# Kernel optimization log

Measured on AMD Instinct MI355X. Metric: run time of the kernel, lower is better.

## Reference

```python
import jax, jax.numpy as jnp
import numpy as np

N_NODES = 200000
N_EDGES = 12800000
C = 5  # channels
RADIUS = 0.05
CONSUME_RADIUS = RADIUS * 2
ACCEL_SCALE = 0.01
MAX_VEL = 0.1
CONSUME_EDGES_REQ = 3
EDGES_TO_STAY_ALIVE = 1
NEG_SLOPE = 0.2  # GATConv leaky_relu slope


def setup_inputs() -> dict:
    key = jax.random.key(0)
    ks = jax.random.split(key, 16)
    x = jax.random.normal(ks[0], (N_NODES, C), dtype=jnp.float32) * 0.1
    # column 4 is node type: 1 = cell, 0 = food
    is_cell = jax.random.bernoulli(ks[1], 0.9, (N_NODES,)).astype(jnp.float32)
    x = x.at[:, 4].set(is_cell)
    edge_index = jax.random.randint(ks[2], (2, N_EDGES), 0, N_NODES, dtype=jnp.int32)
    # edge_attr: [distance, is_cell_edge]
    dist = jax.random.uniform(ks[3], (N_EDGES,), dtype=jnp.float32) * 0.2
    cell_edge = jax.random.bernoulli(ks[4], 0.8, (N_EDGES,)).astype(jnp.float32)
    edge_attr = jnp.stack([dist, cell_edge], axis=1)
    s = 1.0 / np.sqrt(C)
    W = jax.random.normal(ks[5], (C, C), dtype=jnp.float32) * s        # GAT lin (shared src/dst)
    att_src = jax.random.normal(ks[6], (C,), dtype=jnp.float32) * s
    att_dst = jax.random.normal(ks[7], (C,), dtype=jnp.float32) * s
    We = jax.random.normal(ks[8], (2, C), dtype=jnp.float32) * 0.7      # lin_edge
    att_edge = jax.random.normal(ks[9], (C,), dtype=jnp.float32) * s
    gat_bias = jnp.zeros((C,), dtype=jnp.float32)
    W1 = jax.random.normal(ks[10], (C, C), dtype=jnp.float32) * s
    b1 = jnp.zeros((C,), dtype=jnp.float32)
    W2 = jax.random.normal(ks[11], (C, 2), dtype=jnp.float32) * s
    b2 = jnp.zeros((2,), dtype=jnp.float32)
    return {"x": x, "edge_index": edge_index, "edge_attr": edge_attr,
            "W": W, "att_src": att_src, "att_dst": att_dst, "We": We,
            "att_edge": att_edge, "gat_bias": gat_bias,
            "W1": W1, "b1": b1, "W2": W2, "b2": b2}


def _gat_conv(x, edge_index, edge_attr, W, att_src, att_dst, We, att_edge, gat_bias):
    # PyG GATConv, heads=1, edge_dim=2: softmax over incoming edges of each dst node
    n = x.shape[0]
    src, dst = edge_index[0], edge_index[1]
    hs = x @ W                                   # [N, C]
    a_src = hs @ att_src                         # [N]
    a_dst = hs @ att_dst                         # [N]
    a_e = (edge_attr @ We) @ att_edge            # [E]
    logits = jax.nn.leaky_relu(a_src[src] + a_dst[dst] + a_e, NEG_SLOPE)  # [E]
    m = jax.ops.segment_max(logits, dst, num_segments=n)                  # [N]
    ev = jnp.exp(logits - m[dst])
    denom = jax.ops.segment_sum(ev, dst, num_segments=n)                  # [N]
    alpha = ev / jnp.maximum(denom, 1e-16)[dst]
    out = jax.ops.segment_sum(hs[src] * alpha[:, None], dst, num_segments=n)
    return out + gat_bias


def reference(x, edge_index, edge_attr, W, att_src, att_dst, We, att_edge, gat_bias, W1, b1, W2, b2):
    n = x.shape[0]
    src = edge_index[0]
    # convolve: GAT -> MLP -> *2-1
    h = _gat_conv(x, edge_index, edge_attr, W, att_src, att_dst, We, att_edge, gat_bias)
    h = jax.nn.relu(jax.nn.relu(h @ W1 + b1) @ W2 + b2)
    h = h * 2.0 - 1.0                             # [N, 2]
    # only cells (type==1) accelerate
    food_mask = (x[:, 4] == 1).astype(jnp.float32)
    accel = h * ACCEL_SCALE * food_mask[:, None]
    velocity = jnp.clip(x[:, 2:4] + accel, -MAX_VEL, MAX_VEL)
    positions = x[:, :2] + velocity
    new_x = jnp.concatenate([positions, velocity, x[:, 4:]], axis=1)  # [N, 5]
    # border cost
    eps = 1e-6
    out_mask = (jnp.abs(positions) > 1).astype(jnp.float32)
    border_cost = jnp.sum(jnp.log(jnp.abs(positions) + eps) * out_mask)
    # consume-food mask: food nodes with >=3 close edges
    close = (edge_attr[:, 0] < CONSUME_RADIUS).astype(jnp.int32)
    close_cnt = jax.ops.segment_sum(close, src, num_segments=n)
    consumed = (x[:, 4] == 0) & (close_cnt >= CONSUME_EDGES_REQ)
    # island-cell mask: cells with < 1 cell-edge
    cell_e = (edge_attr[:, 1] == 1).astype(jnp.int32)
    cell_cnt = jax.ops.segment_sum(cell_e, src, num_segments=n)
    dead = (x[:, 4] == 1) & (cell_cnt < EDGES_TO_STAY_ALIVE)
    return (new_x, jnp.mean(jnp.abs(velocity), axis=0), border_cost,
            jnp.sum(consumed.astype(jnp.int32)), jnp.sum(dead.astype(jnp.int32)))
```

## Files before the change

kernel.cpp:

```cpp
#include <hip/hip_runtime.h>
#include <math.h>

#define NEG_SLOPE   0.2f
#define CONSUME_R   0.1f
#define ACCEL_SCALE 0.01f
#define MAX_VEL     0.1f

#define NBUCK  2048
#define TPB    512
#define EPT    16
#define EPB    (TPB*EPT)
#define MAXNPB 128
#define SMAX   6912

typedef float    v2f __attribute__((ext_vector_type(2)));
typedef unsigned v2u __attribute__((ext_vector_type(2)));

__device__ __forceinline__ unsigned bucket_of(unsigned v, unsigned npb, float inv_npb,
                                              unsigned* loc)
{
    unsigned b = (unsigned)((float)v * inv_npb);
    unsigned lo = b * npb;
    if (v < lo)            { --b; lo -= npb; }
    else if (v >= lo + npb){ ++b; lo += npb; }
    *loc = v - lo;
    return b;
}

__global__ __launch_bounds__(256) void k_pre(
    const float* __restrict__ x, const float* __restrict__ W,
    const float* __restrict__ att_src, const float* __restrict__ att_dst,
    uint4* __restrict__ npack, float* __restrict__ aD, int n)
{
    int i = blockIdx.x * 256 + threadIdx.x;
    if (i >= n) return;
    float xr[5];
#pragma unroll
    for (int k = 0; k < 5; ++k) xr[k] = x[(size_t)i * 5 + k];
    float hs[5];
#pragma unroll
    for (int c = 0; c < 5; ++c) {
        float s = 0.f;
#pragma unroll
        for (int k = 0; k < 5; ++k) s += xr[k] * W[k * 5 + c];
        hs[c] = s;
    }
    float a_s = 0.f, a_d = 0.f;
#pragma unroll
    for (int c = 0; c < 5; ++c) { a_s += hs[c] * att_src[c]; a_d += hs[c] * att_dst[c]; }
    aD[i] = a_d;
    unsigned b[5];
#pragma unroll
    for (int c = 0; c < 5; ++c) {
        unsigned u = __float_as_uint(hs[c]);
        b[c] = (u + 0x7FFFu + ((u >> 16) & 1u)) >> 16;
    }
    npack[i] = make_uint4(b[0] | (b[1] << 16), b[2] | (b[3] << 16), b[4],
                          __float_as_uint(a_s));
}

__global__ __launch_bounds__(TPB) void k_hist(
    const int* __restrict__ dst, int* __restrict__ hist,
    int NB, int nE, unsigned npb, float inv_npb)
{
    __shared__ int hd[NBUCK];
    int t = threadIdx.x, blk = blockIdx.x;
    for (int j = t; j < NBUCK; j += TPB) hd[j] = 0;
    __syncthreads();
    int base = blk * EPB;
#pragma unroll 4
    for (int k = 0; k < EPT; ++k) {
        int e = base + k * TPB + t;
        if (e < nE) {
            unsigned loc;
            unsigned bd = bucket_of((unsigned)__builtin_nontemporal_load(dst + e),
                                    npb, inv_npb, &loc);
            atomicAdd(&hd[bd], 1);
        }
    }
    __syncthreads();
    for (int j = t; j < NBUCK; j += TPB) hist[(size_t)blk * NBUCK + j] = hd[j];
}

__global__ __launch_bounds__(256) void k_scanA(
    int* __restrict__ hist, int* __restrict__ rowtot, int NB)
{
    int b = blockIdx.x, t = threadIdx.x;
    __shared__ int ws4[4];
    __shared__ int carry;
    if (t == 0) carry = 0;
    __syncthreads();
    for (int base = 0; base < NB; base += 256) {
        int i = base + t;
        int v = (i < NB) ? hist[(size_t)i * NBUCK + b] : 0;
        int xv = v;
#pragma unroll
        for (int off = 1; off < 64; off <<= 1) {
            int y = __shfl_up(xv, off);
            if ((t & 63) >= off) xv += y;
        }
        if ((t & 63) == 63) ws4[t >> 6] = xv;
        __syncthreads();
        int add = 0;
        for (int w = 0; w < (t >> 6); ++w) add += ws4[w];
        int total = ws4[0] + ws4[1] + ws4[2] + ws4[3];
        if (i < NB) hist[(size_t)i * NBUCK + b] = carry + xv + add - v;
        __syncthreads();
        if (t == 0) carry += total;
        __syncthreads();
    }
    if (t == 0) rowtot[b] = carry;
}

__global__ __launch_bounds__(1024) void k_scanB(
    const int* __restrict__ rowtot, int* __restrict__ bbase)
{
    __shared__ int wsum[16], wex[16];
    int t = threadIdx.x;
    int a = rowtot[2 * t], b2 = rowtot[2 * t + 1];
    int v = a + b2;
    int xv = v;
#pragma unroll
    for (int off = 1; off < 64; off <<= 1) {
        int y = __shfl_up(xv, off);
        if ((t & 63) >= off) xv += y;
    }
    if ((t & 63) == 63) wsum[t >> 6] = xv;
    __syncthreads();
    if (t == 0) { int r = 0; for (int w = 0; w < 16; ++w) { wex[w] = r; r += wsum[w]; } }
    __syncthreads();
    int excl = xv - v + wex[t >> 6];
    bbase[2 * t] = excl;
    bbase[2 * t + 1] = excl + a;
    if (t == 1023) bbase[NBUCK] = excl + v;
}

__global__ __launch_bounds__(TPB) void k_scatter(
    const int* __restrict__ ei, const float* __restrict__ ea,
    const float* __restrict__ We, const float* __restrict__ att_edge,
    const int* __restrict__ hist, const int* __restrict__ bbase,
    unsigned* __restrict__ payD, unsigned short* __restrict__ payS,
    int* __restrict__ dirS, int NB, int nE, unsigned npb, float inv_npb)
{
    __shared__ int cD[NBUCK], cS[NBUCK], baseS[NBUCK], dirGl[NBUCK];
    __shared__ unsigned short paySL[EPB];
    __shared__ int wsc[8], wex[8];
    int t = threadIdx.x, blk = blockIdx.x;
    for (int j = t; j < NBUCK; j += TPB) {
        cD[j] = 0; cS[j] = 0;
        dirGl[j] = bbase[j] + hist[(size_t)blk * NBUCK + j];
    }
    __syncthreads();

    float v0 = 0.f, v1 = 0.f;
#pragma unroll
    for (int c = 0; c < 5; ++c) { v0 += We[c] * att_edge[c]; v1 += We[5 + c] * att_edge[c]; }

    int base = blk * EPB;
    unsigned key[EPT], bb[EPT];
    float ae[EPT];

#pragma unroll
    for (int k = 0; k < EPT; ++k) {
        int e = base + k * TPB + t;
        bb[k] = 0;
        if (e < nE) {
            unsigned s = (unsigned)__builtin_nontemporal_load(ei + e);
            unsigned d = (unsigned)__builtin_nontemporal_load(ei + nE + e);
            v2f at = __builtin_nontemporal_load((const v2f*)ea + e);
            unsigned dloc, sloc;
            unsigned bd = bucket_of(d, npb, inv_npb, &dloc);
            unsigned bs = bucket_of(s, npb, inv_npb, &sloc);
            ae[k]  = at.x * v0 + at.y * v1;
            key[k] = s | (dloc << 18);
            bool close = at.x < CONSUME_R;
            bool cell  = (at.y == 1.0f);
            bb[k] = bd | (bs << 11) | (close ? (1u << 22) : 0u)
                       | (cell ? (1u << 23) : 0u) | (1u << 24);
            if (close || cell) atomicAdd(&cS[bs], 1);
        }
    }
    __syncthreads();

    {
        int a0 = cS[4 * t], a1 = cS[4 * t + 1], a2 = cS[4 * t + 2], a3 = cS[4 * t + 3];
        int lsum = a0 + a1 + a2 + a3;
        int xv = lsum;
#pragma unroll
        for (int off = 1; off < 64; off <<= 1) {
            int y = __shfl_up(xv, off);
            if ((t & 63) >= off) xv += y;
        }
        if ((t & 63) == 63) wsc[t >> 6] = xv;
        __syncthreads();
        if (t == 0) { int r = 0; for (int w = 0; w < 8; ++w) { wex[w] = r; r += wsc[w]; } }
        __syncthreads();
        int b0 = xv - lsum + wex[t >> 6];
        baseS[4 * t]     = b0;
        baseS[4 * t + 1] = b0 + a0;
        baseS[4 * t + 2] = b0 + a0 + a1;
        baseS[4 * t + 3] = b0 + a0 + a1 + a2;
    }
    __syncthreads();
    for (int j = t; j < NBUCK; j += TPB) {
        dirS[(size_t)blk * NBUCK + j] = baseS[j] | (cS[j] << 16);
        cS[j] = 0;
    }
    __syncthreads();

#pragma unroll
    for (int k = 0; k < EPT; ++k) {
        if (bb[k] & (1u << 24)) {
            unsigned bd = bb[k] & 0x7FFu;
            int r = atomicAdd(&cD[bd], 1);
            v2u rec; rec.x = key[k]; rec.y = __float_as_uint(ae[k]);
            ((v2u*)payD)[dirGl[bd] + r] = rec;
            if (bb[k] & 0xC00000u) {
                unsigned bs = (bb[k] >> 11) & 0x7FFu;
                unsigned sloc = (key[k] & 0x3FFFFu) - bs * npb;
                unsigned srec = sloc | ((bb[k] >> 22) & 1u) << 11 | ((bb[k] >> 23) & 1u) << 12;
                int r2 = atomicAdd(&cS[bs], 1);
                paySL[baseS[bs] + r2] = (unsigned short)srec;
            }
        }
    }
    __syncthreads();

    unsigned* pgs = (unsigned*)(payS + (size_t)blk * EPB);
    const unsigned* pls = (const unsigned*)paySL;
#pragma unroll
    for (int j = 0; j < EPB / 2 / TPB; ++j) pgs[j * TPB + t] = pls[j * TPB + t];
}

__global__ __launch_bounds__(1024) void k_sortred(
    const unsigned* __restrict__ payD, const unsigned short* __restrict__ payS,
    const int* __restrict__ bbase, const int* __restrict__ dirS,
    const uint4* __restrict__ npack, const float* __restrict__ aD,
    const float* __restrict__ x,
    const float* __restrict__ gat_bias, const float* __restrict__ W1,
    const float* __restrict__ b1, const float* __restrict__ W2,
    const float* __restrict__ b2,
    float* __restrict__ out, float* __restrict__ scal,
    int NB, int n, int npb)
{
    __shared__ unsigned srt[SMAX * 2];
    __shared__ float accf[MAXNPB * 6];
    __shared__ float aDl[MAXNPB];
    __shared__ int cntL[MAXNPB], offL[MAXNPB], cnts[MAXNPB];
    __shared__ float sm[16][5];

    int b = blockIdx.x, t = threadIdx.x;
    int lo = bbase[b], hi = bbase[b + 1], span = hi - lo;
    int first = b * npb;
    int nodes = n - first; if (nodes > npb) nodes = npb; if (nodes < 0) nodes = 0;

    for (int j = t; j < npb; j += 1024) { cntL[j] = 0; cnts[j] = 0; }
    for (int j = t; j < npb * 6; j += 1024) accf[j] = 0.f;
    for (int j = t; j < nodes; j += 1024) aDl[j] = aD[first + j];
    __syncthreads();

    int grp = t >> 4, l16 = t & 15;

    if (span <= SMAX) {
        for (int idx = lo + t; idx < hi; idx += 1024) {
            unsigned w0 = __builtin_nontemporal_load(payD + 2 * (size_t)idx);
            atomicAdd(&cntL[(w0 >> 18) & 0x3FFu], 1);
        }
        __syncthreads();
        if (t == 0) {
            int r = 0;
            for (int j = 0; j < nodes; ++j) { offL[j] = r; r += cntL[j]; cntL[j] = 0; }
        }
        __syncthreads();
        for (int idx = lo + t; idx < hi; idx += 1024) {
            v2u rec = *((const v2u*)payD + idx);
            unsigned dl = (rec.x >> 18) & 0x3FFu;
            int r = atomicAdd(&cntL[dl], 1);
            int p = offL[dl] + r;
            srt[2 * p] = rec.x; srt[2 * p + 1] = rec.y;
        }
        __syncthreads();
        for (int nd = grp; nd < nodes; nd += 64) {
            int s = offL[nd], e = s + cntL[nd];
            float s0 = 0.f, s1 = 0.f, s2 = 0.f, s3 = 0.f, s4 = 0.f, s5 = 0.f;
            for (int j = s + l16; j < e; j += 16) {
                unsigned w0 = srt[2 * j];
                float aev = __uint_as_float(srt[2 * j + 1]);
                uint4 hp = npack[w0 & 0x3FFFFu];
                float z = __uint_as_float(hp.w) + aev + aDl[nd];
                float l = z > 0.f ? z : NEG_SLOPE * z;
                float ev = __expf(l);
                s0 += ev * __uint_as_float(hp.x << 16);
                s1 += ev * __uint_as_float(hp.x & 0xFFFF0000u);
                s2 += ev * __uint_as_float(hp.y << 16);
                s3 += ev * __uint_as_float(hp.y & 0xFFFF0000u);
                s4 += ev * __uint_as_float(hp.z << 16);
                s5 += ev;
            }
#pragma unroll
            for (int m = 1; m < 16; m <<= 1) {
                s0 += __shfl_xor(s0, m);
                s1 += __shfl_xor(s1, m);
                s2 += __shfl_xor(s2, m);
                s3 += __shfl_xor(s3, m);
                s4 += __shfl_xor(s4, m);
                s5 += __shfl_xor(s5, m);
            }
            if (l16 == 0) {
                float* a = &accf[nd * 6];
                a[0] += s0; a[1] += s1; a[2] += s2; a[3] += s3; a[4] += s4; a[5] += s5;
            }
        }
    } else {
        for (int idx = lo + t; idx < hi; idx += 1024) {
            v2u rec = *((const v2u*)payD + idx);
            unsigned dl = (rec.x >> 18) & 0x3FFu;
            uint4 hp = npack[rec.x & 0x3FFFFu];
            float z = __uint_as_float(hp.w) + __uint_as_float(rec.y) + aDl[dl];
            float l = z > 0.f ? z : NEG_SLOPE * z;
            float ev = __expf(l);
            float* a = &accf[dl * 6];
            atomicAdd(a + 0, ev * __uint_as_float(hp.x << 16));
            atomicAdd(a + 1, ev * __uint_as_float(hp.x & 0xFFFF0000u));
            atomicAdd(a + 2, ev * __uint_as_float(hp.y << 16));
            atomicAdd(a + 3, ev * __uint_as_float(hp.y & 0xFFFF0000u));
            atomicAdd(a + 4, ev * __uint_as_float(hp.z << 16));
            atomicAdd(a + 5, ev);
        }
    }

    for (int s = grp; s < NB; s += 64) {
        int pk = dirS[(size_t)s * NBUCK + b];
        int st = pk & 0xFFFF, cn = ((unsigned)pk) >> 16;
        size_t sb = (size_t)s * EPB;
        for (int j = st + l16; j < st + cn; j += 16) {
            unsigned sr = payS[sb + j];
            int add = (int)((sr >> 11) & 1u) | (int)(((sr >> 12) & 1u) << 16);
            atomicAdd(&cnts[sr & 0x3FFu], add);
        }
    }
    __syncthreads();

    float part[5] = {0.f, 0.f, 0.f, 0.f, 0.f};
    if (t < nodes) {
        int i = first + t;
        const float* a = &accf[t * 6];
        float inv = 1.0f / fmaxf(a[5], 1e-16f);
        float h[5];
#pragma unroll
        for (int c = 0; c < 5; ++c) h[c] = a[c] * inv + gat_bias[c];
        float tt[5];
#pragma unroll
        for (int c = 0; c < 5; ++c) {
            float s = b1[c];
#pragma unroll
            for (int k = 0; k < 5; ++k) s += h[k] * W1[k * 5 + c];
            tt[c] = fmaxf(s, 0.f);
        }
        float u0 = b2[0], u1 = b2[1];
#pragma unroll
        for (int k = 0; k < 5; ++k) { u0 += tt[k] * W2[k * 2]; u1 += tt[k] * W2[k * 2 + 1]; }
        u0 = fmaxf(u0, 0.f) * 2.f - 1.f;
        u1 = fmaxf(u1, 0.f) * 2.f - 1.f;

        float px = x[(size_t)i * 5],     py = x[(size_t)i * 5 + 1];
        float vx = x[(size_t)i * 5 + 2], vy = x[(size_t)i * 5 + 3];
        float ty = x[(size_t)i * 5 + 4];
        float mask = (ty == 1.0f) ? 1.0f : 0.0f;
        float nvx = fminf(fmaxf(vx + u0 * ACCEL_SCALE * mask, -MAX_VEL), MAX_VEL);
        float nvy = fminf(fmaxf(vy + u1 * ACCEL_SCALE * mask, -MAX_VEL), MAX_VEL);
        float npx = px + nvx, npy = py + nvy;

        out[(size_t)i * 5]     = npx;
        out[(size_t)i * 5 + 1] = npy;
        out[(size_t)i * 5 + 2] = nvx;
        out[(size_t)i * 5 + 3] = nvy;
        out[(size_t)i * 5 + 4] = ty;

        part[0] = fabsf(nvx);
        part[1] = fabsf(nvy);
        float bc = 0.f;
        if (fabsf(npx) > 1.0f) bc += logf(fabsf(npx) + 1e-6f);
        if (fabsf(npy) > 1.0f) bc += logf(fabsf(npy) + 1e-6f);
        part[2] = bc;
        int c = cnts[t];
        part[3] = (ty == 0.0f && (c & 0xffff) >= 3) ? 1.f : 0.f;
        part[4] = (ty == 1.0f && (c >> 16) < 1) ? 1.f : 0.f;
    }

#pragma unroll
    for (int q = 0; q < 5; ++q)
#pragma unroll
        for (int off = 32; off > 0; off >>= 1)
            part[q] += __shfl_down(part[q], off);
    int lane = t & 63, wid = t >> 6;
    if (lane == 0)
#pragma unroll
        for (int q = 0; q < 5; ++q) sm[wid][q] = part[q];
    __syncthreads();
    if (t == 0) {
#pragma unroll
        for (int q = 0; q < 5; ++q) {
            float s = 0.f;
#pragma unroll
            for (int w = 0; w < 16; ++w) s += sm[w][q];
            unsafeAtomicAdd(scal + q, s);
        }
    }
}

__global__ void k_tail(const float* __restrict__ scal, float* __restrict__ out, int n)
{
    if (threadIdx.x == 0 && blockIdx.x == 0) {
        size_t base = (size_t)n * 5;
        float invn = 1.0f / (float)n;
        out[base + 0] = scal[0] * invn;
        out[base + 1] = scal[1] * invn;
        out[base + 2] = scal[2];
        out[base + 3] = scal[3];
        out[base + 4] = scal[4];
    }
}

__global__ __launch_bounds__(256) void k_node_pre_fb(
    const float* __restrict__ x, const float* __restrict__ W,
    const float* __restrict__ att_src, const float* __restrict__ att_dst,
    float* __restrict__ npack, int n)
{
    int i = blockIdx.x * 256 + threadIdx.x;
    if (i >= n) return;
    float xr[5];
#pragma unroll
    for (int k = 0; k < 5; ++k) xr[k] = x[(size_t)i * 5 + k];
    float hs[5];
#pragma unroll
    for (int c = 0; c < 5; ++c) {
        float s = 0.f;
#pragma unroll
        for (int k = 0; k < 5; ++k) s += xr[k] * W[k * 5 + c];
        hs[c] = s;
    }
    float a_s = 0.f, a_d = 0.f;
#pragma unroll
    for (int c = 0; c < 5; ++c) { a_s += hs[c] * att_src[c]; a_d += hs[c] * att_dst[c]; }
    *(float4*)(npack + (size_t)i * 8)     = make_float4(hs[0], hs[1], hs[2], hs[3]);
    *(float4*)(npack + (size_t)i * 8 + 4) = make_float4(hs[4], a_s, a_d, 0.f);
}

__global__ __launch_bounds__(256) void k_edge_fb(
    const int* __restrict__ ei, const float* __restrict__ ea,
    const float* __restrict__ We, const float* __restrict__ att_edge,
    const float* __restrict__ npack, float* __restrict__ acc,
    int* __restrict__ cnt, int nE)
{
    int e = blockIdx.x * 256 + threadIdx.x;
    if (e >= nE) return;
    float v0 = 0.f, v1 = 0.f;
#pragma unroll
    for (int c = 0; c < 5; ++c) { v0 += We[c] * att_edge[c]; v1 += We[5 + c] * att_edge[c]; }
    int s = ei[e];
    int d = ei[nE + e];
    float2 at = *(const float2*)(ea + (size_t)e * 2);
    const float4 p0 = *(const float4*)(npack + (size_t)s * 8);
    const float2 p1 = *(const float2*)(npack + (size_t)s * 8 + 4);
    float a_dst_d = npack[(size_t)d * 8 + 6];
    float z = p1.y + a_dst_d + (at.x * v0 + at.y * v1);
    float l = z > 0.f ? z : NEG_SLOPE * z;
    float ev = __expf(l);
    float* ad = acc + (size_t)d * 8;
    unsafeAtomicAdd(ad + 0, ev * p0.x);
    unsafeAtomicAdd(ad + 1, ev * p0.y);
    unsafeAtomicAdd(ad + 2, ev * p0.z);
    unsafeAtomicAdd(ad + 3, ev * p0.w);
    unsafeAtomicAdd(ad + 4, ev * p1.x);
    unsafeAtomicAdd(ad + 5, ev);
    int cb = (at.x < CONSUME_R ? 1 : 0) | (at.y == 1.0f ? (1 << 16) : 0);
    if (cb) atomicAdd(cnt + s, cb);
}

__global__ __launch_bounds__(256) void k_final_fb(
    const float* __restrict__ x, const float* __restrict__ acc,
    const int* __restrict__ cnt,
    const float* __restrict__ gat_bias, const float* __restrict__ W1,
    const float* __restrict__ b1, const float* __restrict__ W2,
    const float* __restrict__ b2,
    float* __restrict__ out, float* __restrict__ scal, int n)
{
    int i = blockIdx.x * 256 + threadIdx.x;
    float part[5] = {0.f, 0.f, 0.f, 0.f, 0.f};
    if (i < n) {
        const float* a = acc + (size_t)i * 8;
        float inv = 1.0f / fmaxf(a[5], 1e-16f);
        float h[5];
#pragma unroll
        for (int c = 0; c < 5; ++c) h[c] = a[c] * inv + gat_bias[c];
        float tt[5];
#pragma unroll
        for (int c = 0; c < 5; ++c) {
            float s = b1[c];
#pragma unroll
            for (int k = 0; k < 5; ++k) s += h[k] * W1[k * 5 + c];
            tt[c] = fmaxf(s, 0.f);
        }
        float u0 = b2[0], u1 = b2[1];
#pragma unroll
        for (int k = 0; k < 5; ++k) { u0 += tt[k] * W2[k * 2]; u1 += tt[k] * W2[k * 2 + 1]; }
        u0 = fmaxf(u0, 0.f) * 2.f - 1.f;
        u1 = fmaxf(u1, 0.f) * 2.f - 1.f;
        float px = x[(size_t)i * 5],     py = x[(size_t)i * 5 + 1];
        float vx = x[(size_t)i * 5 + 2], vy = x[(size_t)i * 5 + 3];
        float ty = x[(size_t)i * 5 + 4];
        float mask = (ty == 1.0f) ? 1.0f : 0.0f;
        float nvx = fminf(fmaxf(vx + u0 * ACCEL_SCALE * mask, -MAX_VEL), MAX_VEL);
        float nvy = fminf(fmaxf(vy + u1 * ACCEL_SCALE * mask, -MAX_VEL), MAX_VEL);
        float npx = px + nvx, npy = py + nvy;
        out[(size_t)i * 5]     = npx;
        out[(size_t)i * 5 + 1] = npy;
        out[(size_t)i * 5 + 2] = nvx;
        out[(size_t)i * 5 + 3] = nvy;
        out[(size_t)i * 5 + 4] = ty;
        part[0] = fabsf(nvx);
        part[1] = fabsf(nvy);
        float bc = 0.f;
        if (fabsf(npx) > 1.0f) bc += logf(fabsf(npx) + 1e-6f);
        if (fabsf(npy) > 1.0f) bc += logf(fabsf(npy) + 1e-6f);
        part[2] = bc;
        int c = cnt[i];
        part[3] = (ty == 0.0f && (c & 0xffff) >= 3) ? 1.f : 0.f;
        part[4] = (ty == 1.0f && (c >> 16) < 1) ? 1.f : 0.f;
    }
    __shared__ float sm[4][5];
#pragma unroll
    for (int q = 0; q < 5; ++q)
#pragma unroll
        for (int off = 32; off > 0; off >>= 1)
            part[q] += __shfl_down(part[q], off);
    int lane = threadIdx.x & 63, wid = threadIdx.x >> 6;
    if (lane == 0)
#pragma unroll
        for (int q = 0; q < 5; ++q) sm[wid][q] = part[q];
    __syncthreads();
    if (threadIdx.x == 0) {
#pragma unroll
        for (int q = 0; q < 5; ++q)
            unsafeAtomicAdd(scal + q, sm[0][q] + sm[1][q] + sm[2][q] + sm[3][q]);
    }
}

extern "C" void kernel_launch(void* const* d_in, const int* in_sizes, int n_in,
                              void* d_out, int out_size, void* d_ws, size_t ws_size,
                              hipStream_t stream)
{
    const float* x        = (const float*)d_in[0];
    const int*   ei       = (const int*)  d_in[1];
    const float* ea       = (const float*)d_in[2];
    const float* W        = (const float*)d_in[3];
    const float* att_src  = (const float*)d_in[4];
    const float* att_dst  = (const float*)d_in[5];
    const float* We       = (const float*)d_in[6];
    const float* att_edge = (const float*)d_in[7];
    const float* gat_bias = (const float*)d_in[8];
    const float* b1       = (const float*)d_in[10];
    const float* W1       = (const float*)d_in[9];
    const float* W2       = (const float*)d_in[11];
    const float* b2       = (const float*)d_in[12];

    int n  = in_sizes[0] / 5;
    int nE = in_sizes[1] / 2;

    int npb = (n + NBUCK - 1) / NBUCK;
    int NB = (nE + EPB - 1) / EPB;
    float inv_npb = 1.0f / (float)npb;

    size_t o = 0;
    auto alloc = [&](size_t bytes) { size_t r = o; o = (o + bytes + 63) & ~63ULL; return r; };
    size_t off_npack = alloc((size_t)n * 16);
    size_t off_aD    = alloc((size_t)n * 4);
    size_t off_hist  = alloc((size_t)NB * NBUCK * 4);
    size_t off_rtot  = alloc((size_t)NBUCK * 4);
    size_t off_bbase = alloc((size_t)(NBUCK + 1) * 4);
    size_t off_dirS  = alloc((size_t)NB * NBUCK * 4);
    size_t off_payS  = alloc((size_t)NB * EPB * 2);
    size_t off_scal  = alloc(64);
    size_t off_payD  = alloc((size_t)nE * 8);
    size_t need = o;

    char* wsb = (char*)d_ws;
    bool ok_shape = (n < (1 << 18)) && (npb <= MAXNPB) && (NB >= 1);
    bool fast = ok_shape && (ws_size >= need);

    if (fast) {
        uint4*          npack = (uint4*)(wsb + off_npack);
        float*          aD    = (float*)(wsb + off_aD);
        int*            hist  = (int*)(wsb + off_hist);
        int*            rtot  = (int*)(wsb + off_rtot);
        int*            bbase = (int*)(wsb + off_bbase);
        int*            dirS  = (int*)(wsb + off_dirS);
        unsigned short* payS  = (unsigned short*)(wsb + off_payS);
        float*          scal  = (float*)(wsb + off_scal);
        unsigned*       payD  = (unsigned*)(wsb + off_payD);

        hipMemsetAsync(scal, 0, 64, stream);
        k_pre<<<(n + 255) / 256, 256, 0, stream>>>(x, W, att_src, att_dst, npack, aD, n);
        k_hist<<<NB, TPB, 0, stream>>>(ei + nE, hist, NB, nE, (unsigned)npb, inv_npb);
        k_scanA<<<NBUCK, 256, 0, stream>>>(hist, rtot, NB);
        k_scanB<<<1, 1024, 0, stream>>>(rtot, bbase);
        k_scatter<<<NB, TPB, 0, stream>>>(ei, ea, We, att_edge, hist, bbase,
                                          payD, payS, dirS, NB, nE, (unsigned)npb, inv_npb);
        k_sortred<<<NBUCK, 1024, 0, stream>>>(payD, payS, bbase, dirS, npack, aD, x,
                                              gat_bias, W1, b1, W2, b2,
                                              (float*)d_out, scal, NB, n, npb);
        k_tail<<<1, 64, 0, stream>>>(scal, (float*)d_out, n);
    } else {
        float* ws    = (float*)d_ws;
        float* npk   = ws;
        float* acc   = ws + (size_t)n * 8;
        int*   cnt   = (int*)(acc + (size_t)n * 8);
        float* scal  = (float*)(cnt + n);
        size_t zbytes = ((size_t)n * 8 + (size_t)n + 8) * sizeof(float);
        hipMemsetAsync(acc, 0, zbytes, stream);
        k_node_pre_fb<<<(n + 255) / 256, 256, 0, stream>>>(x, W, att_src, att_dst, npk, n);
        k_edge_fb<<<(nE + 255) / 256, 256, 0, stream>>>(ei, ea, We, att_edge, npk,
                                                        acc, cnt, nE);
        k_final_fb<<<(n + 255) / 256, 256, 0, stream>>>(x, acc, cnt, gat_bias, W1, b1,
                                                        W2, b2, (float*)d_out, scal, n);
        k_tail<<<1, 64, 0, stream>>>(scal, (float*)d_out, n);
    }
}
```

Baseline: 695.7 us.

## Replace source-bucket sort with global atomic counters and drop LDS per-node sort

The scatter kernel no longer builds a second per-block source-bucketed payload and directory. It instead counts close and cell edges per source node with global atomics into a packed int counter array, which k_pre now zeroes in place of the memset. The reduction kernel drops the shared-memory counting sort by destination and always accumulates with LDS float atomics. This removes several passes, extra traffic and synchronisation, but adds heavy global atomic contention (about 12.8M atomics over 200k nodes) and LDS atomic contention per destination node.

```diff
diff --git a/kernel.cpp b/kernel.cpp
--- a/kernel.cpp
+++ b/kernel.cpp
@@ -11,7 +11,6 @@
 #define EPT    16
 #define EPB    (TPB*EPT)
 #define MAXNPB 128
-#define SMAX   6912
 
 typedef float    v2f __attribute__((ext_vector_type(2)));
 typedef unsigned v2u __attribute__((ext_vector_type(2)));
@@ -30,10 +29,13 @@
 __global__ __launch_bounds__(256) void k_pre(
     const float* __restrict__ x, const float* __restrict__ W,
     const float* __restrict__ att_src, const float* __restrict__ att_dst,
-    uint4* __restrict__ npack, float* __restrict__ aD, int n)
+    uint4* __restrict__ npack, float* __restrict__ aD,
+    int* __restrict__ cnt, float* __restrict__ scal, int n)
 {
     int i = blockIdx.x * 256 + threadIdx.x;
     if (i >= n) return;
+    cnt[i] = 0;
+    if (i < 8) scal[i] = 0.f;
     float xr[5];
 #pragma unroll
     for (int k = 0; k < 5; ++k) xr[k] = x[(size_t)i * 5 + k];
@@ -139,15 +141,13 @@
     const int* __restrict__ ei, const float* __restrict__ ea,
     const float* __restrict__ We, const float* __restrict__ att_edge,
     const int* __restrict__ hist, const int* __restrict__ bbase,
-    unsigned* __restrict__ payD, unsigned short* __restrict__ payS,
-    int* __restrict__ dirS, int NB, int nE, unsigned npb, float inv_npb)
-{
-    __shared__ int cD[NBUCK], cS[NBUCK], baseS[NBUCK], dirGl[NBUCK];
-    __shared__ unsigned short paySL[EPB];
-    __shared__ int wsc[8], wex[8];
+    unsigned* __restrict__ payD, int* __restrict__ cnt,
+    int nE, unsigned npb, float inv_npb)
+{
+    __shared__ int cD[NBUCK], dirGl[NBUCK];
     int t = threadIdx.x, blk = blockIdx.x;
     for (int j = t; j < NBUCK; j += TPB) {
-        cD[j] = 0; cS[j] = 0;
+        cD[j] = 0;
         dirGl[j] = bbase[j] + hist[(size_t)blk * NBUCK + j];
     }
     __syncthreads();
@@ -157,187 +157,62 @@
     for (int c = 0; c < 5; ++c) { v0 += We[c] * att_edge[c]; v1 += We[5 + c] * att_edge[c]; }
 
     int base = blk * EPB;
-    unsigned key[EPT], bb[EPT];
-    float ae[EPT];
-
 #pragma unroll
     for (int k = 0; k < EPT; ++k) {
         int e = base + k * TPB + t;
-        bb[k] = 0;
         if (e < nE) {
             unsigned s = (unsigned)__builtin_nontemporal_load(ei + e);
             unsigned d = (unsigned)__builtin_nontemporal_load(ei + nE + e);
             v2f at = __builtin_nontemporal_load((const v2f*)ea + e);
-            unsigned dloc, sloc;
+            unsigned dloc;
             unsigned bd = bucket_of(d, npb, inv_npb, &dloc);
-            unsigned bs = bucket_of(s, npb, inv_npb, &sloc);
-            ae[k]  = at.x * v0 + at.y * v1;
-            key[k] = s | (dloc << 18);
-            bool close = at.x < CONSUME_R;
-            bool cell  = (at.y == 1.0f);
-            bb[k] = bd | (bs << 11) | (close ? (1u << 22) : 0u)
-                       | (cell ? (1u << 23) : 0u) | (1u << 24);
-            if (close || cell) atomicAdd(&cS[bs], 1);
+            float aev = at.x * v0 + at.y * v1;
+            int r = atomicAdd(&cD[bd], 1);
+            v2u rec; rec.x = s | (dloc << 18); rec.y = __float_as_uint(aev);
+            ((v2u*)payD)[dirGl[bd] + r] = rec;
+            int cb = (at.x < CONSUME_R ? 1 : 0) | (at.y == 1.0f ? (1 << 16) : 0);
+            if (cb) atomicAdd(cnt + (int)s, cb);
         }
     }
-    __syncthreads();
-
-    {
-        int a0 = cS[4 * t], a1 = cS[4 * t + 1], a2 = cS[4 * t + 2], a3 = cS[4 * t + 3];
-        int lsum = a0 + a1 + a2 + a3;
-        int xv = lsum;
-#pragma unroll
-        for (int off = 1; off < 64; off <<= 1) {
-            int y = __shfl_up(xv, off);
-            if ((t & 63) >= off) xv += y;
-        }
-        if ((t & 63) == 63) wsc[t >> 6] = xv;
-        __syncthreads();
-        if (t == 0) { int r = 0; for (int w = 0; w < 8; ++w) { wex[w] = r; r += wsc[w]; } }
-        __syncthreads();
-        int b0 = xv - lsum + wex[t >> 6];
-        baseS[4 * t]     = b0;
-        baseS[4 * t + 1] = b0 + a0;
-        baseS[4 * t + 2] = b0 + a0 + a1;
-        baseS[4 * t + 3] = b0 + a0 + a1 + a2;
-    }
-    __syncthreads();
-    for (int j = t; j < NBUCK; j += TPB) {
-        dirS[(size_t)blk * NBUCK + j] = baseS[j] | (cS[j] << 16);
-        cS[j] = 0;
-    }
-    __syncthreads();
-
-#pragma unroll
-    for (int k = 0; k < EPT; ++k) {
-        if (bb[k] & (1u << 24)) {
-            unsigned bd = bb[k] & 0x7FFu;
-            int r = atomicAdd(&cD[bd], 1);
-            v2u rec; rec.x = key[k]; rec.y = __float_as_uint(ae[k]);
-            ((v2u*)payD)[dirGl[bd] + r] = rec;
-            if (bb[k] & 0xC00000u) {
-                unsigned bs = (bb[k] >> 11) & 0x7FFu;
-                unsigned sloc = (key[k] & 0x3FFFFu) - bs * npb;
-                unsigned srec = sloc | ((bb[k] >> 22) & 1u) << 11 | ((bb[k] >> 23) & 1u) << 12;
-                int r2 = atomicAdd(&cS[bs], 1);
-                paySL[baseS[bs] + r2] = (unsigned short)srec;
-            }
-        }
-    }
-    __syncthreads();
-
-    unsigned* pgs = (unsigned*)(payS + (size_t)blk * EPB);
-    const unsigned* pls = (const unsigned*)paySL;
-#pragma unroll
-    for (int j = 0; j < EPB / 2 / TPB; ++j) pgs[j * TPB + t] = pls[j * TPB + t];
-}
-
-__global__ __launch_bounds__(1024) void k_sortred(
-    const unsigned* __restrict__ payD, const unsigned short* __restrict__ payS,
-    const int* __restrict__ bbase, const int* __restrict__ dirS,
+}
+
+__global__ __launch_bounds__(1024) void k_red(
+    const unsigned* __restrict__ payD, const int* __restrict__ bbase,
     const uint4* __restrict__ npack, const float* __restrict__ aD,
-    const float* __restrict__ x,
+    const float* __restrict__ x, const int* __restrict__ cnt,
     const float* __restrict__ gat_bias, const float* __restrict__ W1,
     const float* __restrict__ b1, const float* __restrict__ W2,
     const float* __restrict__ b2,
     float* __restrict__ out, float* __restrict__ scal,
-    int NB, int n, int npb)
-{
-    __shared__ unsigned srt[SMAX * 2];
+    int n, int npb)
+{
     __shared__ float accf[MAXNPB * 6];
     __shared__ float aDl[MAXNPB];
-    __shared__ int cntL[MAXNPB], offL[MAXNPB], cnts[MAXNPB];
     __shared__ float sm[16][5];
 
     int b = blockIdx.x, t = threadIdx.x;
-    int lo = bbase[b], hi = bbase[b + 1], span = hi - lo;
+    int lo = bbase[b], hi = bbase[b + 1];
     int first = b * npb;
     int nodes = n - first; if (nodes > npb) nodes = npb; if (nodes < 0) nodes = 0;
 
-    for (int j = t; j < npb; j += 1024) { cntL[j] = 0; cnts[j] = 0; }
     for (int j = t; j < npb * 6; j += 1024) accf[j] = 0.f;
     for (int j = t; j < nodes; j += 1024) aDl[j] = aD[first + j];
     __syncthreads();
 
-    int grp = t >> 4, l16 = t & 15;
-
-    if (span <= SMAX) {
-        for (int idx = lo + t; idx < hi; idx += 1024) {
-            unsigned w0 = __builtin_nontemporal_load(payD + 2 * (size_t)idx);
-            atomicAdd(&cntL[(w0 >> 18) & 0x3FFu], 1);
-        }
-        __syncthreads();
-        if (t == 0) {
-            int r = 0;
-            for (int j = 0; j < nodes; ++j) { offL[j] = r; r += cntL[j]; cntL[j] = 0; }
-        }
-        __syncthreads();
-        for (int idx = lo + t; idx < hi; idx += 1024) {
-            v2u rec = *((const v2u*)payD + idx);
-            unsigned dl = (rec.x >> 18) & 0x3FFu;
-            int r = atomicAdd(&cntL[dl], 1);
-            int p = offL[dl] + r;
-            srt[2 * p] = rec.x; srt[2 * p + 1] = rec.y;
-        }
-        __syncthreads();
-        for (int nd = grp; nd < nodes; nd += 64) {
-            int s = offL[nd], e = s + cntL[nd];
-            float s0 = 0.f, s1 = 0.f, s2 = 0.f, s3 = 0.f, s4 = 0.f, s5 = 0.f;
-            for (int j = s + l16; j < e; j += 16) {
-                unsigned w0 = srt[2 * j];
-                float aev = __uint_as_float(srt[2 * j + 1]);
-                uint4 hp = npack[w0 & 0x3FFFFu];
-                float z = __uint_as_float(hp.w) + aev + aDl[nd];
-                float l = z > 0.f ? z : NEG_SLOPE * z;
-                float ev = __expf(l);
-                s0 += ev * __uint_as_float(hp.x << 16);
-                s1 += ev * __uint_as_float(hp.x & 0xFFFF0000u);
-                s2 += ev * __uint_as_float(hp.y << 16);
-                s3 += ev * __uint_as_float(hp.y & 0xFFFF0000u);
-                s4 += ev * __uint_as_float(hp.z << 16);
-                s5 += ev;
-            }
-#pragma unroll
-            for (int m = 1; m < 16; m <<= 1) {
-                s0 += __shfl_xor(s0, m);
-                s1 += __shfl_xor(s1, m);
-                s2 += __shfl_xor(s2, m);
-                s3 += __shfl_xor(s3, m);
-                s4 += __shfl_xor(s4, m);
-                s5 += __shfl_xor(s5, m);
-            }
-            if (l16 == 0) {
-                float* a = &accf[nd * 6];
-                a[0] += s0; a[1] += s1; a[2] += s2; a[3] += s3; a[4] += s4; a[5] += s5;
-            }
-        }
-    } else {
-        for (int idx = lo + t; idx < hi; idx += 1024) {
-            v2u rec = *((const v2u*)payD + idx);
-            unsigned dl = (rec.x >> 18) & 0x3FFu;
-            uint4 hp = npack[rec.x & 0x3FFFFu];
-            float z = __uint_as_float(hp.w) + __uint_as_float(rec.y) + aDl[dl];
-            float l = z > 0.f ? z : NEG_SLOPE * z;
-            float ev = __expf(l);
-            float* a = &accf[dl * 6];
-            atomicAdd(a + 0, ev * __uint_as_float(hp.x << 16));
-            atomicAdd(a + 1, ev * __uint_as_float(hp.x & 0xFFFF0000u));
-            atomicAdd(a + 2, ev * __uint_as_float(hp.y << 16));
-            atomicAdd(a + 3, ev * __uint_as_float(hp.y & 0xFFFF0000u));
-            atomicAdd(a + 4, ev * __uint_as_float(hp.z << 16));
-            atomicAdd(a + 5, ev);
-        }
-    }
-
-    for (int s = grp; s < NB; s += 64) {
-        int pk = dirS[(size_t)s * NBUCK + b];
-        int st = pk & 0xFFFF, cn = ((unsigned)pk) >> 16;
-        size_t sb = (size_t)s * EPB;
-        for (int j = st + l16; j < st + cn; j += 16) {
-            unsigned sr = payS[sb + j];
-            int add = (int)((sr >> 11) & 1u) | (int)(((sr >> 12) & 1u) << 16);
-            atomicAdd(&cnts[sr & 0x3FFu], add);
-        }
+#pragma unroll 2
+    for (int idx = lo + t; idx < hi; idx += 1024) {
+        v2u rec = __builtin_nontemporal_load((const v2u*)payD + idx);
+        unsigned dl = (rec.x >> 18) & 0x3FFu;
+        uint4 hp = npack[rec.x & 0x3FFFFu];
+        float z = __uint_as_float(hp.w) + __uint_as_float(rec.y) + aDl[dl];
+        float l = fmaxf(z, NEG_SLOPE * z);
+        float ev = __expf(l);
+        atomicAdd(&accf[dl * 6 + 0], ev * __uint_as_float(hp.x << 16));
+        atomicAdd(&accf[dl * 6 + 1], ev * __uint_as_float(hp.x & 0xFFFF0000u));
+        atomicAdd(&accf[dl * 6 + 2], ev * __uint_as_float(hp.y << 16));
+        atomicAdd(&accf[dl * 6 + 3], ev * __uint_as_float(hp.y & 0xFFFF0000u));
+        atomicAdd(&accf[dl * 6 + 4], ev * __uint_as_float(hp.z << 16));
+        atomicAdd(&accf[dl * 6 + 5], ev);
     }
     __syncthreads();
 
@@ -383,9 +258,9 @@
         if (fabsf(npx) > 1.0f) bc += logf(fabsf(npx) + 1e-6f);
         if (fabsf(npy) > 1.0f) bc += logf(fabsf(npy) + 1e-6f);
         part[2] = bc;
-        int c = cnts[t];
+        int c = cnt[i];
         part[3] = (ty == 0.0f && (c & 0xffff) >= 3) ? 1.f : 0.f;
-        part[4] = (ty == 1.0f && (c >> 16) < 1) ? 1.f : 0.f;
+        part[4] = (ty == 1.0f && ((c >> 16) & 0xffff) < 1) ? 1.f : 0.f;
     }
 
 #pragma unroll
@@ -579,8 +454,7 @@
     size_t off_hist  = alloc((size_t)NB * NBUCK * 4);
     size_t off_rtot  = alloc((size_t)NBUCK * 4);
     size_t off_bbase = alloc((size_t)(NBUCK + 1) * 4);
-    size_t off_dirS  = alloc((size_t)NB * NBUCK * 4);
-    size_t off_payS  = alloc((size_t)NB * EPB * 2);
+    size_t off_cnt   = alloc((size_t)n * 4);
     size_t off_scal  = alloc(64);
     size_t off_payD  = alloc((size_t)nE * 8);
     size_t need = o;
@@ -595,21 +469,20 @@
         int*            hist  = (int*)(wsb + off_hist);
         int*            rtot  = (int*)(wsb + off_rtot);
         int*            bbase = (int*)(wsb + off_bbase);
-        int*            dirS  = (int*)(wsb + off_dirS);
-        unsigned short* payS  = (unsigned short*)(wsb + off_payS);
+        int*            cnt   = (int*)(wsb + off_cnt);
         float*          scal  = (float*)(wsb + off_scal);
         unsigned*       payD  = (unsigned*)(wsb + off_payD);
 
-        hipMemsetAsync(scal, 0, 64, stream);
-        k_pre<<<(n + 255) / 256, 256, 0, stream>>>(x, W, att_src, att_dst, npack, aD, n);
+        k_pre<<<(n + 255) / 256, 256, 0, stream>>>(x, W, att_src, att_dst, npack, aD,
+                                                   cnt, scal, n);
         k_hist<<<NB, TPB, 0, stream>>>(ei + nE, hist, NB, nE, (unsigned)npb, inv_npb);
         k_scanA<<<NBUCK, 256, 0, stream>>>(hist, rtot, NB);
         k_scanB<<<1, 1024, 0, stream>>>(rtot, bbase);
         k_scatter<<<NB, TPB, 0, stream>>>(ei, ea, We, att_edge, hist, bbase,
-                                          payD, payS, dirS, NB, nE, (unsigned)npb, inv_npb);
-        k_sortred<<<NBUCK, 1024, 0, stream>>>(payD, payS, bbase, dirS, npack, aD, x,
-                                              gat_bias, W1, b1, W2, b2,
-                                              (float*)d_out, scal, NB, n, npb);
+                                          payD, cnt, nE, (unsigned)npb, inv_npb);
+        k_red<<<NBUCK, 1024, 0, stream>>>(payD, bbase, npack, aD, x, cnt,
+                                          gat_bias, W1, b1, W2, b2,
+                                          (float*)d_out, scal, n, npb);
         k_tail<<<1, 64, 0, stream>>>(scal, (float*)d_out, n);
     } else {
         float* ws    = (float*)d_ws;
```

Measured after the change: 1.232 ms. 1.77x slower.
